# Kernel tuning notes

Measured on AMD Instinct MI355X. Metric: run time of the kernel, lower is better.

## Reference

```python
import jax, jax.numpy as jnp
import numpy as np

VOCAB, D, H1, H2, T = 32000, 256, 256, 256, 12
PAD, START, STOP = 0, 10, 11
B, S, NS = 32, 512, 16


def setup_inputs() -> dict:
    key = jax.random.key(0)
    ks = jax.random.split(key, 16)
    def rn(k, shape, scale=0.1):
        return (jax.random.normal(k, shape) * scale).astype(jnp.float32)
    inputs = jax.random.randint(ks[0], (B, S), 0, VOCAB)
    sent_embs = jax.random.normal(ks[1], (B, NS, 2 * H1), dtype=jnp.float32)
    embed = rn(ks[2], (VOCAB, D)).at[0].set(0.0)  # padding_idx=0
    # BiLSTM 1: input D, hidden H1; gate order i,f,g,o; dim 0 = [fwd, bwd]
    lstm1_wih = rn(ks[3], (2, 4 * H1, D))
    lstm1_whh = rn(ks[4], (2, 4 * H1, H1))
    lstm1_b = rn(ks[5], (2, 4 * H1))  # b_ih + b_hh fused
    # BiLSTM 2: input 4*H1 (= 2*2*lstm1_units), hidden H2
    lstm2_wih = rn(ks[6], (2, 4 * H2, 4 * H1))
    lstm2_whh = rn(ks[7], (2, 4 * H2, H2))
    lstm2_b = rn(ks[8], (2, 4 * H2))
    attW = rn(ks[9], (2 * H1, 2 * H1))
    h2t_w = rn(ks[10], (T, 2 * H2))
    h2t_b = rn(ks[11], (T,))
    trans = jax.random.normal(ks[12], (T, T), dtype=jnp.float32)
    trans = trans.at[START, :].set(-10000.0).at[:, STOP].set(-10000.0)
    return dict(inputs=inputs, sent_embs=sent_embs, embed=embed,
                lstm1_wih=lstm1_wih, lstm1_whh=lstm1_whh, lstm1_b=lstm1_b,
                lstm2_wih=lstm2_wih, lstm2_whh=lstm2_whh, lstm2_b=lstm2_b,
                attW=attW, h2t_w=h2t_w, h2t_b=h2t_b, trans=trans)


def _lstm_dir(x, wih, whh, b, reverse=False):
    # x: (S, B, Din) -> (S, B, H)
    if reverse:
        x = x[::-1]
    Hh = whh.shape[1]
    Bn = x.shape[1]
    def step(carry, xt):
        h, c = carry
        gates = xt @ wih.T + h @ whh.T + b
        i, f, g, o = jnp.split(gates, 4, axis=-1)
        c = jax.nn.sigmoid(f) * c + jax.nn.sigmoid(i) * jnp.tanh(g)
        h = jax.nn.sigmoid(o) * jnp.tanh(c)
        return (h, c), h
    init = (jnp.zeros((Bn, Hh), x.dtype), jnp.zeros((Bn, Hh), x.dtype))
    _, hs = jax.lax.scan(step, init, x)
    return hs[::-1] if reverse else hs


def _bilstm(x, wih, whh, b):
    fwd = _lstm_dir(x, wih[0], whh[0], b[0])
    bwd = _lstm_dir(x, wih[1], whh[1], b[1], reverse=True)
    return jnp.concatenate([fwd, bwd], axis=-1)


def _lstm_features(inputs, sent_embs, embed, lstm1_wih, lstm1_whh, lstm1_b,
                   lstm2_wih, lstm2_whh, lstm2_b, attW, h2t_w, h2t_b):
    emb = embed[inputs].transpose(1, 0, 2)            # (S,B,D); dropout is identity at eval
    l1 = _bilstm(emb, lstm1_wih, lstm1_whh, lstm1_b)  # (S,B,2H1)
    word = l1.transpose(1, 0, 2)                      # (B,S,2H1)
    wx = jnp.einsum('bse,fe->bsf', word, attW)        # Linear W (no bias)
    scores = jnp.einsum('bsf,bnf->bsn', wx, sent_embs)
    aw = jax.nn.softmax(scores, axis=-1)
    g = jnp.einsum('bsn,bnf->bsf', aw, sent_embs)
    comb = jnp.concatenate([wx, g], axis=-1)          # (B,S,4H1)
    l2 = _bilstm(comb.transpose(1, 0, 2), lstm2_wih, lstm2_whh, lstm2_b)  # (S,B,2H2)
    feats = jnp.einsum('sbf,tf->bst', l2, h2t_w) + h2t_b  # (B,S,T)
    return feats


def _viterbi(feats_b, trans):
    # feats_b: (S,T) -> (path (S,), score)
    init = jnp.full((T,), -10000.0, feats_b.dtype).at[START].set(0.0)
    def step(fv, feat):
        sc = fv[None, :] + trans          # [next, prev]
        bp = jnp.argmax(sc, axis=1)
        return jnp.max(sc, axis=1) + feat, bp
    fv, bps = jax.lax.scan(step, init, feats_b)
    term = fv + trans[STOP]
    best = jnp.argmax(term)
    def back(tag, bp):
        return bp[tag], tag
    _, path = jax.lax.scan(back, best, bps, reverse=True)
    return path, term[best]


def reference(inputs, sent_embs, embed, lstm1_wih, lstm1_whh, lstm1_b,
              lstm2_wih, lstm2_whh, lstm2_b, attW, h2t_w, h2t_b, trans):
    feats = _lstm_features(inputs, sent_embs, embed, lstm1_wih, lstm1_whh, lstm1_b,
                           lstm2_wih, lstm2_whh, lstm2_b, attW, h2t_w, h2t_b)
    paths, _ = jax.vmap(_viterbi, in_axes=(0, None))(feats, trans)
    return paths  # (B,S) predicted tag sequence
```

## Files before the change

kernel.cpp:

```cpp
#include <hip/hip_runtime.h>
#include <hip/hip_bf16.h>

#define BB 32
#define SS 512
#define DD 256
#define HH 256
#define GG 1024
#define MM (SS*BB)
#define NSENT 16
#define TT 12
#define TAG_START 10
#define TAG_STOP 11

typedef unsigned long long u64;
typedef unsigned int u32;

__device__ __forceinline__ float sigm(float x) {
  x = fminf(fmaxf(x, -15.f), 15.f);
  return 1.f / (1.f + __expf(-x));
}
__device__ __forceinline__ float tanh_fast(float x) {
  x = fminf(fmaxf(x, -15.f), 15.f);
  float e = __expf(2.f * x);
  return (e - 1.f) / (e + 1.f);
}

__global__ void embed_kernel(const int* __restrict__ toks, const float* __restrict__ emb,
                             float* __restrict__ X1) {
  int m = blockIdx.x;
  int s = m >> 5, b = m & 31;
  int tok = toks[b * SS + s];
  ((float4*)(X1 + (size_t)m * DD))[threadIdx.x] =
      ((const float4*)(emb + (size_t)tok * DD))[threadIdx.x];
}

__launch_bounds__(256)
__global__ void gemm_nt(const float* __restrict__ A, const float* __restrict__ W_,
                        const float* __restrict__ bias_, float* __restrict__ C_,
                        int K, int lda, int ldw, int ldC, size_t wz, size_t cz) {
  __shared__ float As[16 * 132];
  __shared__ float Ws[16 * 132];
  const float* W = W_ + (size_t)blockIdx.z * wz;
  const float* bias = bias_ ? bias_ + (size_t)blockIdx.z * GG : nullptr;
  float* C = C_ + (size_t)blockIdx.z * cz;
  const int tid = threadIdx.x;
  const int n0 = blockIdx.x * 128, m0 = blockIdx.y * 128;
  const int row = tid & 127, half = tid >> 7;
  const int tx = tid & 15, ty = tid >> 4;
  float acc[8][8] = {};
  const float* Arow = A + (size_t)(m0 + row) * lda;
  const float* Wrow = W + (size_t)(n0 + row) * ldw;
  for (int kk = 0; kk < K; kk += 16) {
    const int kb = half * 8;
    float4 a0 = *(const float4*)(Arow + kk + kb);
    float4 a1 = *(const float4*)(Arow + kk + kb + 4);
    float4 w0 = *(const float4*)(Wrow + kk + kb);
    float4 w1 = *(const float4*)(Wrow + kk + kb + 4);
    As[(kb + 0) * 132 + row] = a0.x; As[(kb + 1) * 132 + row] = a0.y;
    As[(kb + 2) * 132 + row] = a0.z; As[(kb + 3) * 132 + row] = a0.w;
    As[(kb + 4) * 132 + row] = a1.x; As[(kb + 5) * 132 + row] = a1.y;
    As[(kb + 6) * 132 + row] = a1.z; As[(kb + 7) * 132 + row] = a1.w;
    Ws[(kb + 0) * 132 + row] = w0.x; Ws[(kb + 1) * 132 + row] = w0.y;
    Ws[(kb + 2) * 132 + row] = w0.z; Ws[(kb + 3) * 132 + row] = w0.w;
    Ws[(kb + 4) * 132 + row] = w1.x; Ws[(kb + 5) * 132 + row] = w1.y;
    Ws[(kb + 6) * 132 + row] = w1.z; Ws[(kb + 7) * 132 + row] = w1.w;
    __syncthreads();
#pragma unroll
    for (int kl = 0; kl < 16; ++kl) {
      const float4 alo = *(const float4*)&As[kl * 132 + ty * 4];
      const float4 ahi = *(const float4*)&As[kl * 132 + 64 + ty * 4];
      const float4 wlo = *(const float4*)&Ws[kl * 132 + tx * 4];
      const float4 whi = *(const float4*)&Ws[kl * 132 + 64 + tx * 4];
      const float am[8] = {alo.x, alo.y, alo.z, alo.w, ahi.x, ahi.y, ahi.z, ahi.w};
      const float wm[8] = {wlo.x, wlo.y, wlo.z, wlo.w, whi.x, whi.y, whi.z, whi.w};
#pragma unroll
      for (int i = 0; i < 8; ++i)
#pragma unroll
        for (int j = 0; j < 8; ++j) acc[i][j] = fmaf(am[i], wm[j], acc[i][j]);
    }
    __syncthreads();
  }
  float4 blo = make_float4(0.f, 0.f, 0.f, 0.f), bhi = blo;
  if (bias) {
    blo = *(const float4*)(bias + n0 + tx * 4);
    bhi = *(const float4*)(bias + n0 + 64 + tx * 4);
  }
#pragma unroll
  for (int i = 0; i < 8; ++i) {
    const int m = m0 + ((i < 4) ? (ty * 4 + i) : (64 + ty * 4 + i - 4));
    float4 lo = make_float4(acc[i][0] + blo.x, acc[i][1] + blo.y,
                            acc[i][2] + blo.z, acc[i][3] + blo.w);
    float4 hi = make_float4(acc[i][4] + bhi.x, acc[i][5] + bhi.y,
                            acc[i][6] + bhi.z, acc[i][7] + bhi.w);
    *(float4*)(C + (size_t)m * ldC + n0 + tx * 4) = lo;
    *(float4*)(C + (size_t)m * ldC + n0 + 64 + tx * 4) = hi;
  }
}

__global__ void prep_whh(const float* __restrict__ whh1, const float* __restrict__ whh2,
                         float* __restrict__ o1, float* __restrict__ o2) {
  int idx0 = blockIdx.x * 256 + threadIdx.x;
  int layer = idx0 >> 19;
  int idx = idx0 & 524287;
  const float* whh = layer ? whh2 : whh1;
  float* out = layer ? o2 : o1;
  int c    = idx & 3;
  int t    = (idx >> 2) & 255;
  int i4   = (idx >> 10) & 31;
  int sl   = (idx >> 15) & 7;
  int d    = idx >> 18;
  int r    = t & 127;
  int half = t >> 7;
  int g = (r >> 5) * 256 + sl * 32 + (r & 31);
  int k = half * 128 + i4 * 4 + c;
  out[idx] = whh[(size_t)(d * GG + g) * HH + k];
}

__launch_bounds__(256, 1)
__global__ void rec_kernel(const float* __restrict__ Xp, const float* __restrict__ whh_p,
                           float* __restrict__ hist, u64* __restrict__ hx,
                           const float* __restrict__ aw, const float* __restrict__ sentW,
                           int useAtt) {
  __shared__ float h_lds[512];
  __shared__ float p_lds[512];
  const int tid = threadIdx.x;
  const int bid = blockIdx.x;
  const int sl = bid >> 5;
  const int db = bid & 31;
  const int d = db & 1;
  const int bg = db >> 1;
  const int r = tid & 127;
  const int half = tid >> 7;
  const float* wp = whh_p + (size_t)(d * 8 + sl) * 32768;
  float w[128];
#pragma unroll
  for (int i4 = 0; i4 < 32; ++i4) {
    const float4 v = *(const float4*)&wp[(size_t)(i4 * 256 + tid) * 4];
    w[i4 * 4 + 0] = v.x; w[i4 * 4 + 1] = v.y;
    w[i4 * 4 + 2] = v.z; w[i4 * 4 + 3] = v.w;
  }
  const float* XpD = Xp + (size_t)d * MM * GG;
  const int gcol = (r >> 5) * 256 + sl * 32 + (r & 31);
  const int jj = tid & 31, cc = tid >> 5;
  const int histMine = ((r >> 4) == sl);
  float creg = 0.f;
  float swA[8], swB[8];
  if (useAtt) {
    const float* swp = sentW + ((size_t)d * 512 + (size_t)(bg * 2) * 16) * 1024 + gcol;
#pragma unroll
    for (int n = 0; n < 8; ++n) {
      swA[n] = swp[(size_t)(half * 8 + n) * 1024];
      swB[n] = swp[(size_t)(16 + half * 8 + n) * 1024];
    }
  }
  u64* grp[2] = { hx + ((size_t)(0 * 2 + d) * 16 + bg) * 512,
                  hx + ((size_t)(1 * 2 + d) * 16 + bg) * 512 };
#pragma unroll 1
  for (int t = 0; t < SS; ++t) {
    const int s = d ? (SS - 1 - t) : t;
    const int m0 = s * BB + bg * 2;
    float x0 = 0.f, x1 = 0.f;
    if (half == 0) {
      x0 = XpD[(size_t)m0 * GG + gcol];
      x1 = XpD[(size_t)(m0 + 1) * GG + gcol];
    }
    if (useAtt) {
      const float* a0 = aw + (size_t)m0 * 16;
#pragma unroll
      for (int n = 0; n < 8; ++n) {
        x0 = fmaf(a0[half * 8 + n], swA[n], x0);
        x1 = fmaf(a0[16 + half * 8 + n], swB[n], x1);
      }
    }
    u64 w0, w1;
    {
      u64* base = grp[t & 1] + tid * 2;
      w0 = __hip_atomic_load(base + 0, __ATOMIC_RELAXED, __HIP_MEMORY_SCOPE_AGENT);
      w1 = __hip_atomic_load(base + 1, __ATOMIC_RELAXED, __HIP_MEMORY_SCOPE_AGENT);
      while (((u32)(w0 >> 32) != (u32)t) | ((u32)(w1 >> 32) != (u32)t)) {
        __builtin_amdgcn_s_sleep(1);
        w0 = __hip_atomic_load(base + 0, __ATOMIC_RELAXED, __HIP_MEMORY_SCOPE_AGENT);
        w1 = __hip_atomic_load(base + 1, __ATOMIC_RELAXED, __HIP_MEMORY_SCOPE_AGENT);
      }
    }
    *(float2*)&h_lds[tid * 2] = make_float2(__uint_as_float((u32)w0),
                                            __uint_as_float((u32)w1));
    __syncthreads();
    {
      const int kb = half * 128;
      float p0a = 0.f, p0b = 0.f, p1a = 0.f, p1b = 0.f;
#pragma unroll
      for (int k8 = 0; k8 < 16; ++k8) {
        const float4 h0a = *(const float4*)&h_lds[kb + k8 * 8];
        const float4 h0b = *(const float4*)&h_lds[kb + k8 * 8 + 4];
        const float4 h1a = *(const float4*)&h_lds[256 + kb + k8 * 8];
        const float4 h1b = *(const float4*)&h_lds[256 + kb + k8 * 8 + 4];
        p0a = fmaf(w[k8*8+0], h0a.x, p0a); p0a = fmaf(w[k8*8+1], h0a.y, p0a);
        p0a = fmaf(w[k8*8+2], h0a.z, p0a); p0a = fmaf(w[k8*8+3], h0a.w, p0a);
        p0b = fmaf(w[k8*8+4], h0b.x, p0b); p0b = fmaf(w[k8*8+5], h0b.y, p0b);
        p0b = fmaf(w[k8*8+6], h0b.z, p0b); p0b = fmaf(w[k8*8+7], h0b.w, p0b);
        p1a = fmaf(w[k8*8+0], h1a.x, p1a); p1a = fmaf(w[k8*8+1], h1a.y, p1a);
        p1a = fmaf(w[k8*8+2], h1a.z, p1a); p1a = fmaf(w[k8*8+3], h1a.w, p1a);
        p1b = fmaf(w[k8*8+4], h1b.x, p1b); p1b = fmaf(w[k8*8+5], h1b.y, p1b);
        p1b = fmaf(w[k8*8+6], h1b.z, p1b); p1b = fmaf(w[k8*8+7], h1b.w, p1b);
      }
      *(float2*)&p_lds[tid * 2] = make_float2(p0a + p0b + x0, p1a + p1b + x1);
    }
    __syncthreads();
    if (tid < 64) {
      const float iv = p_lds[(jj) * 2 + cc]       + p_lds[(128 + jj) * 2 + cc];
      const float fv = p_lds[(32 + jj) * 2 + cc]  + p_lds[(128 + 32 + jj) * 2 + cc];
      const float gv = p_lds[(64 + jj) * 2 + cc]  + p_lds[(128 + 64 + jj) * 2 + cc];
      const float ov = p_lds[(96 + jj) * 2 + cc]  + p_lds[(128 + 96 + jj) * 2 + cc];
      const float cs = sigm(fv) * creg + sigm(iv) * tanh_fast(gv);
      creg = cs;
      const float hn = sigm(ov) * tanh_fast(cs);
      u64 wv = ((u64)(u32)(t + 1) << 32) | (u64)__float_as_uint(hn);
      __hip_atomic_store(grp[(t + 1) & 1] + cc * 256 + sl * 32 + jj, wv,
                         __ATOMIC_RELAXED, __HIP_MEMORY_SCOPE_AGENT);
    }
    if (histMine && t > 0) {
      const int sp = d ? (SS - t) : (t - 1);
      *(float2*)&hist[(size_t)(sp * BB + bg * 2 + half) * 512 + d * 256 + r * 2] =
          make_float2(__uint_as_float((u32)w0), __uint_as_float((u32)w1));
    }
  }
  if (histMine) {
    u64* base = grp[SS & 1] + tid * 2;
    u64 w0, w1;
    do {
      w0 = __hip_atomic_load(base + 0, __ATOMIC_RELAXED, __HIP_MEMORY_SCOPE_AGENT);
      w1 = __hip_atomic_load(base + 1, __ATOMIC_RELAXED, __HIP_MEMORY_SCOPE_AGENT);
      if (((u32)(w0 >> 32) == (u32)SS) & ((u32)(w1 >> 32) == (u32)SS)) break;
      __builtin_amdgcn_s_sleep(1);
    } while (true);
    const int sp = d ? 0 : (SS - 1);
    *(float2*)&hist[(size_t)(sp * BB + bg * 2 + half) * 512 + d * 256 + r * 2] =
        make_float2(__uint_as_float((u32)w0), __uint_as_float((u32)w1));
  }
}

__global__ void aw_kernel(const float* __restrict__ wx, const float* __restrict__ sent,
                          float* __restrict__ awout) {
  __shared__ float sl[NSENT * 512];
  __shared__ float wxr[512];
  __shared__ float parts[256];
  __shared__ float avals[NSENT];
  __shared__ float red0;
  const int tid = threadIdx.x;
  const int b = blockIdx.y;
  const int s0 = blockIdx.x * 32;
  for (int i = tid; i < NSENT * 512; i += 256) sl[i] = sent[(size_t)b * NSENT * 512 + i];
  __syncthreads();
  for (int si = 0; si < 32; ++si) {
    const int m = (s0 + si) * BB + b;
    for (int i = tid; i < 512; i += 256) wxr[i] = wx[(size_t)m * 512 + i];
    __syncthreads();
    const int n = tid >> 4, kp = tid & 15;
    float p = 0.f;
#pragma unroll 8
    for (int f = kp * 32; f < kp * 32 + 32; ++f) p = fmaf(wxr[f], sl[n * 512 + f], p);
    parts[tid] = p;
    __syncthreads();
    if (tid < NSENT) {
      float sc = 0.f;
      for (int qq = 0; qq < 16; ++qq) sc += parts[tid * 16 + qq];
      avals[tid] = sc;
    }
    __syncthreads();
    if (tid == 0) {
      float mx = avals[0];
      for (int qq = 1; qq < NSENT; ++qq) mx = fmaxf(mx, avals[qq]);
      float sm = 0.f;
      for (int qq = 0; qq < NSENT; ++qq) { float e = expf(avals[qq] - mx); avals[qq] = e; sm += e; }
      red0 = 1.f / sm;
    }
    __syncthreads();
    if (tid < NSENT) awout[(size_t)m * 16 + tid] = avals[tid] * red0;
    __syncthreads();
  }
}

__global__ void feats_kernel(const float* __restrict__ l2m, const float* __restrict__ w,
                             const float* __restrict__ bias, float* __restrict__ feats) {
  const int wave = threadIdx.x >> 6, lane = threadIdx.x & 63;
  const int m = blockIdx.x * 4 + wave;
  const float* row = l2m + (size_t)m * 512;
  float rv[8];
#pragma unroll
  for (int i = 0; i < 8; ++i) rv[i] = row[lane + i * 64];
  for (int t = 0; t < TT; ++t) {
    const float* wr = w + t * 512;
    float p = 0.f;
#pragma unroll
    for (int i = 0; i < 8; ++i) p = fmaf(rv[i], wr[lane + i * 64], p);
#pragma unroll
    for (int off = 32; off; off >>= 1) p += __shfl_down(p, off);
    if (lane == 0) feats[(size_t)m * TT + t] = p + bias[t];
  }
}

__global__ void viterbi_kernel(const float* __restrict__ feats, const float* __restrict__ trans,
                               int* __restrict__ out) {
  __shared__ float flds[SS * TT];
  __shared__ unsigned char bp[SS * TT];
  __shared__ float tr[TT * TT];
  __shared__ float fv[TT];
  __shared__ float tv[TT];
  __shared__ int pathS[SS];
  const int b = blockIdx.x, tid = threadIdx.x;
  for (int i = tid; i < SS * TT; i += 64) {
    int s = i / TT, t = i - s * TT;
    flds[i] = feats[(size_t)(s * BB + b) * TT + t];
  }
  for (int i = tid; i < TT * TT; i += 64) tr[i] = trans[i];
  if (tid < TT) fv[tid] = (tid == TAG_START) ? 0.f : -10000.f;
  __syncthreads();
  for (int s = 0; s < SS; ++s) {
    float nf = 0.f;
    if (tid < TT) {
      float mx = -1e30f;
      int bj = 0;
#pragma unroll
      for (int jj = 0; jj < TT; ++jj) {
        float v = fv[jj] + tr[tid * TT + jj];
        if (v > mx) { mx = v; bj = jj; }
      }
      nf = mx + flds[s * TT + tid];
      bp[s * TT + tid] = (unsigned char)bj;
    }
    __syncthreads();
    if (tid < TT) fv[tid] = nf;
    __syncthreads();
  }
  if (tid < TT) tv[tid] = fv[tid] + tr[TAG_STOP * TT + tid];
  __syncthreads();
  if (tid == 0) {
    int best = 0;
    float mx = tv[0];
    for (int jj = 1; jj < TT; ++jj)
      if (tv[jj] > mx) { mx = tv[jj]; best = jj; }
    pathS[SS - 1] = best;
    for (int s = SS - 1; s > 0; --s) { best = bp[s * TT + best]; pathS[s - 1] = best; }
  }
  __syncthreads();
  for (int s = tid; s < SS; s += 64) out[b * SS + s] = pathS[s];
}

#define OFF_XP    ((size_t)0)
#define OFF_WX    ((size_t)134217728)
#define OFF_L2M   ((size_t)167772160)
#define OFF_WORD  ((size_t)201326592)
#define OFF_WT1   ((size_t)234881024)
#define OFF_WT2   ((size_t)236978176)
#define OFF_FEATS ((size_t)239075328)
#define OFF_HX1   ((size_t)239861760)
#define OFF_HX2   ((size_t)240123904)
#define OFF_SENTW ((size_t)240386048)
#define OFF_AW    ((size_t)244580352)

extern "C" void kernel_launch(void* const* d_in, const int* in_sizes, int n_in,
                              void* d_out, int out_size, void* d_ws, size_t ws_size,
                              hipStream_t stream) {
  const int* inputs  = (const int*)d_in[0];
  const float* sent  = (const float*)d_in[1];
  const float* emb   = (const float*)d_in[2];
  const float* l1wih = (const float*)d_in[3];
  const float* l1whh = (const float*)d_in[4];
  const float* l1b   = (const float*)d_in[5];
  const float* l2wih = (const float*)d_in[6];
  const float* l2whh = (const float*)d_in[7];
  const float* l2b   = (const float*)d_in[8];
  const float* attW  = (const float*)d_in[9];
  const float* h2tw  = (const float*)d_in[10];
  const float* h2tb  = (const float*)d_in[11];
  const float* trans = (const float*)d_in[12];
  int* out = (int*)d_out;
  char* ws = (char*)d_ws;

  float* Xp    = (float*)(ws + OFF_XP);
  float* wx    = (float*)(ws + OFF_WX);
  float* l2m   = (float*)(ws + OFF_L2M);
  float* X1    = l2m;
  float* word  = (float*)(ws + OFF_WORD);
  float* wt1   = (float*)(ws + OFF_WT1);
  float* wt2   = (float*)(ws + OFF_WT2);
  float* feats = (float*)(ws + OFF_FEATS);
  u64* hx1     = (u64*)(ws + OFF_HX1);
  u64* hx2     = (u64*)(ws + OFF_HX2);
  float* sentW = (float*)(ws + OFF_SENTW);
  float* awb   = (float*)(ws + OFF_AW);

  (void)hipMemsetAsync(ws + OFF_HX1, 0, 262144 * 2, stream);

  prep_whh<<<4096, 256, 0, stream>>>(l1whh, l2whh, wt1, wt2);
  gemm_nt<<<dim3(8, 4, 2), 256, 0, stream>>>(sent, l2wih + 512, nullptr, sentW,
                                             512, 512, GG, 1024,
                                             (size_t)GG * GG, (size_t)512 * 1024);
  embed_kernel<<<MM, 64, 0, stream>>>(inputs, emb, X1);
  gemm_nt<<<dim3(8, 128, 2), 256, 0, stream>>>(X1, l1wih, l1b, Xp,
                                               DD, DD, DD, GG,
                                               (size_t)GG * DD, (size_t)MM * GG);
  rec_kernel<<<256, 256, 0, stream>>>(Xp, wt1, word, hx1, nullptr, nullptr, 0);
  gemm_nt<<<dim3(4, 128, 1), 256, 0, stream>>>(word, attW, nullptr, wx,
                                               512, 512, 512, 512, 0, 0);
  aw_kernel<<<dim3(16, 32), 256, 0, stream>>>(wx, sent, awb);
  gemm_nt<<<dim3(8, 128, 2), 256, 0, stream>>>(wx, l2wih, l2b, Xp,
                                               512, 512, GG, GG,
                                               (size_t)GG * GG, (size_t)MM * GG);
  rec_kernel<<<256, 256, 0, stream>>>(Xp, wt2, l2m, hx2, awb, sentW, 1);
  feats_kernel<<<MM / 4, 256, 0, stream>>>(l2m, h2tw, h2tb, feats);
  viterbi_kernel<<<BB, 64, 0, stream>>>(feats, trans, out);
}
```

Baseline: 4.075 ms.

## Fold attention weight into layer-2 input projection and use non-coherent spin loads

Precomputes Weff = Wih2[:, :512] @ attW and sent @ attW^T so the big word@attW GEMM over all tokens is removed, and the layer-2 input GEMM and attention scores work directly on the layer-1 output. This cuts one large GEMM's work and its intermediate traffic, at the cost of a few small weight-only GEMMs and a transpose. It also changes the recurrent spin-wait to mostly use raw sc0 loads with a periodic atomic load, and adds a volatile store before the atomic publish. The aim is lower handoff latency between blocks, with some risk around memory visibility.

```diff
diff --git a/kernel.cpp b/kernel.cpp
--- a/kernel.cpp
+++ b/kernel.cpp
@@ -97,6 +97,17 @@
   }
 }
 
+__global__ void transpose512(const float* __restrict__ in, float* __restrict__ out) {
+  __shared__ float tile[32][33];
+  const int bx = blockIdx.x & 15, by = blockIdx.x >> 4;
+  const int tx = threadIdx.x & 31, ty = threadIdx.x >> 5;
+  for (int i = 0; i < 32; i += 8)
+    tile[ty + i][tx] = in[(size_t)(by * 32 + ty + i) * 512 + bx * 32 + tx];
+  __syncthreads();
+  for (int i = 0; i < 32; i += 8)
+    out[(size_t)(bx * 32 + ty + i) * 512 + by * 32 + tx] = tile[tx][ty + i];
+}
+
 __global__ void prep_whh(const float* __restrict__ whh1, const float* __restrict__ whh2,
                          float* __restrict__ o1, float* __restrict__ o2) {
   int idx0 = blockIdx.x * 256 + threadIdx.x;
@@ -175,12 +186,20 @@
     u64 w0, w1;
     {
       u64* base = grp[t & 1] + tid * 2;
-      w0 = __hip_atomic_load(base + 0, __ATOMIC_RELAXED, __HIP_MEMORY_SCOPE_AGENT);
-      w1 = __hip_atomic_load(base + 1, __ATOMIC_RELAXED, __HIP_MEMORY_SCOPE_AGENT);
-      while (((u32)(w0 >> 32) != (u32)t) | ((u32)(w1 >> 32) != (u32)t)) {
+      int spin = 0;
+      for (;;) {
+        if ((spin & 3) == 1) {
+          w0 = __hip_atomic_load(base + 0, __ATOMIC_RELAXED, __HIP_MEMORY_SCOPE_AGENT);
+          w1 = __hip_atomic_load(base + 1, __ATOMIC_RELAXED, __HIP_MEMORY_SCOPE_AGENT);
+        } else {
+          asm volatile("global_load_dwordx2 %0, %2, off sc0\n\t"
+                       "global_load_dwordx2 %1, %2, off offset:8 sc0\n\t"
+                       "s_waitcnt vmcnt(0)"
+                       : "=v"(w0), "=v"(w1) : "v"(base) : "memory");
+        }
+        if (((u32)(w0 >> 32) == (u32)t) & ((u32)(w1 >> 32) == (u32)t)) break;
+        ++spin;
         __builtin_amdgcn_s_sleep(1);
-        w0 = __hip_atomic_load(base + 0, __ATOMIC_RELAXED, __HIP_MEMORY_SCOPE_AGENT);
-        w1 = __hip_atomic_load(base + 1, __ATOMIC_RELAXED, __HIP_MEMORY_SCOPE_AGENT);
       }
     }
     *(float2*)&h_lds[tid * 2] = make_float2(__uint_as_float((u32)w0),
@@ -216,8 +235,9 @@
       creg = cs;
       const float hn = sigm(ov) * tanh_fast(cs);
       u64 wv = ((u64)(u32)(t + 1) << 32) | (u64)__float_as_uint(hn);
-      __hip_atomic_store(grp[(t + 1) & 1] + cc * 256 + sl * 32 + jj, wv,
-                         __ATOMIC_RELAXED, __HIP_MEMORY_SCOPE_AGENT);
+      u64* dst = grp[(t + 1) & 1] + cc * 256 + sl * 32 + jj;
+      *(volatile u64*)dst = wv;
+      __hip_atomic_store(dst, wv, __ATOMIC_RELAXED, __HIP_MEMORY_SCOPE_AGENT);
     }
     if (histMine && t > 0) {
       const int sp = d ? (SS - t) : (t - 1);
@@ -358,6 +378,9 @@
 #define OFF_HX2   ((size_t)240123904)
 #define OFF_SENTW ((size_t)240386048)
 #define OFF_AW    ((size_t)244580352)
+#define OFF_ATTWT (OFF_WX)
+#define OFF_SW    (OFF_WX + (size_t)1048576)
+#define OFF_WEFF  (OFF_WX + (size_t)2097152)
 
 extern "C" void kernel_launch(void* const* d_in, const int* in_sizes, int n_in,
                               void* d_out, int out_size, void* d_ws, size_t ws_size,
@@ -379,7 +402,6 @@
   char* ws = (char*)d_ws;
 
   float* Xp    = (float*)(ws + OFF_XP);
-  float* wx    = (float*)(ws + OFF_WX);
   float* l2m   = (float*)(ws + OFF_L2M);
   float* X1    = l2m;
   float* word  = (float*)(ws + OFF_WORD);
@@ -390,24 +412,33 @@
   u64* hx2     = (u64*)(ws + OFF_HX2);
   float* sentW = (float*)(ws + OFF_SENTW);
   float* awb   = (float*)(ws + OFF_AW);
+  float* attWT = (float*)(ws + OFF_ATTWT);
+  float* SWp   = (float*)(ws + OFF_SW);
+  float* Weff  = (float*)(ws + OFF_WEFF);
 
   (void)hipMemsetAsync(ws + OFF_HX1, 0, 262144 * 2, stream);
 
   prep_whh<<<4096, 256, 0, stream>>>(l1whh, l2whh, wt1, wt2);
+  transpose512<<<256, 256, 0, stream>>>(attW, attWT);
   gemm_nt<<<dim3(8, 4, 2), 256, 0, stream>>>(sent, l2wih + 512, nullptr, sentW,
                                              512, 512, GG, 1024,
                                              (size_t)GG * GG, (size_t)512 * 1024);
+  gemm_nt<<<dim3(4, 8, 1), 256, 0, stream>>>(l2wih, attWT, nullptr, Weff,
+                                             512, GG, 512, 512, 0, 0);
+  gemm_nt<<<dim3(4, 8, 1), 256, 0, stream>>>(l2wih + (size_t)GG * GG, attWT, nullptr,
+                                             Weff + (size_t)1024 * 512,
+                                             512, GG, 512, 512, 0, 0);
+  gemm_nt<<<dim3(4, 4, 1), 256, 0, stream>>>(sent, attWT, nullptr, SWp,
+                                             512, 512, 512, 512, 0, 0);
   embed_kernel<<<MM, 64, 0, stream>>>(inputs, emb, X1);
   gemm_nt<<<dim3(8, 128, 2), 256, 0, stream>>>(X1, l1wih, l1b, Xp,
                                                DD, DD, DD, GG,
                                                (size_t)GG * DD, (size_t)MM * GG);
   rec_kernel<<<256, 256, 0, stream>>>(Xp, wt1, word, hx1, nullptr, nullptr, 0);
-  gemm_nt<<<dim3(4, 128, 1), 256, 0, stream>>>(word, attW, nullptr, wx,
-                                               512, 512, 512, 512, 0, 0);
-  aw_kernel<<<dim3(16, 32), 256, 0, stream>>>(wx, sent, awb);
-  gemm_nt<<<dim3(8, 128, 2), 256, 0, stream>>>(wx, l2wih, l2b, Xp,
-                                               512, 512, GG, GG,
-                                               (size_t)GG * GG, (size_t)MM * GG);
+  aw_kernel<<<dim3(16, 32), 256, 0, stream>>>(word, SWp, awb);
+  gemm_nt<<<dim3(8, 128, 2), 256, 0, stream>>>(word, Weff, l2b, Xp,
+                                               512, 512, 512, GG,
+                                               (size_t)1024 * 512, (size_t)MM * GG);
   rec_kernel<<<256, 256, 0, stream>>>(Xp, wt2, l2m, hx2, awb, sentW, 1);
   feats_kernel<<<MM / 4, 256, 0, stream>>>(l2m, h2tw, h2tb, feats);
   viterbi_kernel<<<BB, 64, 0, stream>>>(feats, trans, out);
```

New measurement: 4.772 ms. 1.17x slower.

## Move attention input term out of recurrence and prefetch next-step input projection

Applied to the files above, without the earlier changes.

The per-step attention contribution (aw weights times sentW) is now added to the precomputed input projection by a separate fully parallel kernel before the second recurrence, instead of being computed serially inside the recurrent loop. The recurrent kernel also prefetches the next timestep's input projection values at the end of each iteration, so the global load latency overlaps with the synchronization wait. This takes work and memory loads off the latency-bound serial critical path, at the cost of an extra pass over the large Xp buffer and one more kernel launch.

```diff
diff --git a/kernel.cpp b/kernel.cpp
--- a/kernel.cpp
+++ b/kernel.cpp
@@ -116,11 +116,34 @@
   out[idx] = whh[(size_t)(d * GG + g) * HH + k];
 }
 
+__global__ void attadd_kernel(const float* __restrict__ aw, const float* __restrict__ sentW,
+                              float* __restrict__ Xp) {
+  __shared__ float a[NSENT];
+  const int idx = blockIdx.x;
+  const int d = idx >> 14;
+  const int m = idx & (MM - 1);
+  const int b = m & 31;
+  const int tid = threadIdx.x;
+  if (tid < NSENT) a[tid] = aw[(size_t)m * 16 + tid];
+  __syncthreads();
+  const int g = tid * 4;
+  float* xp = Xp + ((size_t)d * MM + m) * GG + g;
+  const float* swp = sentW + ((size_t)d * 512 + b * 16) * 1024 + g;
+  float4 acc = *(const float4*)xp;
+#pragma unroll
+  for (int n = 0; n < NSENT; ++n) {
+    const float4 sw = *(const float4*)&swp[(size_t)n * 1024];
+    acc.x = fmaf(a[n], sw.x, acc.x);
+    acc.y = fmaf(a[n], sw.y, acc.y);
+    acc.z = fmaf(a[n], sw.z, acc.z);
+    acc.w = fmaf(a[n], sw.w, acc.w);
+  }
+  *(float4*)xp = acc;
+}
+
 __launch_bounds__(256, 1)
 __global__ void rec_kernel(const float* __restrict__ Xp, const float* __restrict__ whh_p,
-                           float* __restrict__ hist, u64* __restrict__ hx,
-                           const float* __restrict__ aw, const float* __restrict__ sentW,
-                           int useAtt) {
+                           float* __restrict__ hist, u64* __restrict__ hx) {
   __shared__ float h_lds[512];
   __shared__ float p_lds[512];
   const int tid = threadIdx.x;
@@ -144,34 +167,18 @@
   const int jj = tid & 31, cc = tid >> 5;
   const int histMine = ((r >> 4) == sl);
   float creg = 0.f;
-  float swA[8], swB[8];
-  if (useAtt) {
-    const float* swp = sentW + ((size_t)d * 512 + (size_t)(bg * 2) * 16) * 1024 + gcol;
-#pragma unroll
-    for (int n = 0; n < 8; ++n) {
-      swA[n] = swp[(size_t)(half * 8 + n) * 1024];
-      swB[n] = swp[(size_t)(16 + half * 8 + n) * 1024];
-    }
-  }
   u64* grp[2] = { hx + ((size_t)(0 * 2 + d) * 16 + bg) * 512,
                   hx + ((size_t)(1 * 2 + d) * 16 + bg) * 512 };
+  float xn0 = 0.f, xn1 = 0.f;
+  if (half == 0) {
+    const int s0 = d ? (SS - 1) : 0;
+    const int m00 = s0 * BB + bg * 2;
+    xn0 = XpD[(size_t)m00 * GG + gcol];
+    xn1 = XpD[(size_t)(m00 + 1) * GG + gcol];
+  }
 #pragma unroll 1
   for (int t = 0; t < SS; ++t) {
-    const int s = d ? (SS - 1 - t) : t;
-    const int m0 = s * BB + bg * 2;
-    float x0 = 0.f, x1 = 0.f;
-    if (half == 0) {
-      x0 = XpD[(size_t)m0 * GG + gcol];
-      x1 = XpD[(size_t)(m0 + 1) * GG + gcol];
-    }
-    if (useAtt) {
-      const float* a0 = aw + (size_t)m0 * 16;
-#pragma unroll
-      for (int n = 0; n < 8; ++n) {
-        x0 = fmaf(a0[half * 8 + n], swA[n], x0);
-        x1 = fmaf(a0[16 + half * 8 + n], swB[n], x1);
-      }
-    }
+    const float x0 = xn0, x1 = xn1;
     u64 w0, w1;
     {
       u64* base = grp[t & 1] + tid * 2;
@@ -223,6 +230,13 @@
       const int sp = d ? (SS - t) : (t - 1);
       *(float2*)&hist[(size_t)(sp * BB + bg * 2 + half) * 512 + d * 256 + r * 2] =
           make_float2(__uint_as_float((u32)w0), __uint_as_float((u32)w1));
+    }
+    if (half == 0) {
+      const int tn = (t + 1 < SS) ? (t + 1) : (SS - 1);
+      const int sn = d ? (SS - 1 - tn) : tn;
+      const int m0n = sn * BB + bg * 2;
+      xn0 = XpD[(size_t)m0n * GG + gcol];
+      xn1 = XpD[(size_t)(m0n + 1) * GG + gcol];
     }
   }
   if (histMine) {
@@ -401,14 +415,15 @@
   gemm_nt<<<dim3(8, 128, 2), 256, 0, stream>>>(X1, l1wih, l1b, Xp,
                                                DD, DD, DD, GG,
                                                (size_t)GG * DD, (size_t)MM * GG);
-  rec_kernel<<<256, 256, 0, stream>>>(Xp, wt1, word, hx1, nullptr, nullptr, 0);
+  rec_kernel<<<256, 256, 0, stream>>>(Xp, wt1, word, hx1);
   gemm_nt<<<dim3(4, 128, 1), 256, 0, stream>>>(word, attW, nullptr, wx,
                                                512, 512, 512, 512, 0, 0);
   aw_kernel<<<dim3(16, 32), 256, 0, stream>>>(wx, sent, awb);
   gemm_nt<<<dim3(8, 128, 2), 256, 0, stream>>>(wx, l2wih, l2b, Xp,
                                                512, 512, GG, GG,
                                                (size_t)GG * GG, (size_t)MM * GG);
-  rec_kernel<<<256, 256, 0, stream>>>(Xp, wt2, l2m, hx2, awb, sentW, 1);
+  attadd_kernel<<<2 * MM, 256, 0, stream>>>(awb, sentW, Xp);
+  rec_kernel<<<256, 256, 0, stream>>>(Xp, wt2, l2m, hx2);
   feats_kernel<<<MM / 4, 256, 0, stream>>>(l2m, h2tw, h2tb, feats);
   viterbi_kernel<<<BB, 64, 0, stream>>>(feats, trans, out);
 }
```

Measured after the change: 3.910 ms. 1.04x faster.
